# Optimization experiments

Hardware: AMD Instinct MI355X
Metric: run time of the kernel (lower is better)

The kernel has to match this reference:

```python
import jax, jax.numpy as jnp
import numpy as np

BS, S, H, KVH, HD = 4, 4096, 32, 8, 128
BLK = 32                      # tokens per cache page
NB = S // BLK                 # blocks per sequence (128)
NPAGES = BS * NB              # total pages in pool (512)
WIN = 1024                    # sliding window
G = H // KVH                  # query heads per KV head (GQA group)
SCALE = 1.0 / float(np.sqrt(HD))
NEG = -1e30


def setup_inputs() -> dict:
    key = jax.random.key(0)
    k0, k1, k2, k3 = jax.random.split(key, 4)
    q = jax.random.normal(k0, (BS, S, H, HD), dtype=jnp.float32)
    k = jax.random.normal(k1, (BS, S, KVH, HD), dtype=jnp.float32)
    v = jax.random.normal(k2, (BS, S, KVH, HD), dtype=jnp.float32)
    k_cache = jnp.zeros((NPAGES, BLK, KVH, HD), dtype=jnp.float32)
    v_cache = jnp.zeros((NPAGES, BLK, KVH, HD), dtype=jnp.float32)
    # identity block table: page p holds block (p % NB) of sequence (p // NB)
    seq_block_ids = jnp.arange(NPAGES, dtype=jnp.int32).reshape(BS, NB)
    start_positions = jnp.full((BS,), S - 1, dtype=jnp.int32)  # decode last token
    mask = jnp.zeros((BS, 1, 1, S), dtype=jnp.float32)         # additive mask
    sink = jax.random.normal(k3, (H,), dtype=jnp.float32)      # per-head sink logit
    return {"q": q, "k": k, "v": v, "k_cache": k_cache, "v_cache": v_cache,
            "mask": mask, "sink": sink, "seq_block_ids": seq_block_ids,
            "start_positions": start_positions}


def reference(q, k, v, k_cache, v_cache, mask, sink, seq_block_ids, start_positions):
    # ---- prefill: write full k/v into the paged cache ----
    # (the wrapper discards the prefill attention output; cache write is its
    #  only observable effect on the returned decode output)
    kp = k.reshape(BS, NB, BLK, KVH, HD)
    vp = v.reshape(BS, NB, BLK, KVH, HD)
    k_cache = k_cache.at[seq_block_ids].set(kp)
    v_cache = v_cache.at[seq_block_ids].set(vp)

    # ---- decode: write last-token k/v at start_positions ----
    b = jnp.arange(BS)
    pages = seq_block_ids[b, start_positions // BLK]   # [BS]
    offs = start_positions % BLK                       # [BS]
    k_cache = k_cache.at[pages, offs].set(k[:, -1])
    v_cache = v_cache.at[pages, offs].set(v[:, -1])

    # ---- gather cache back into dense [BS, S, KVH, HD] via block table ----
    k_all = k_cache[seq_block_ids].reshape(BS, S, KVH, HD)
    v_all = v_cache[seq_block_ids].reshape(BS, S, KVH, HD)

    # ---- last-token paged attention with sliding window + sink ----
    q_last = q[:, -1].reshape(BS, KVH, G, HD)          # group query heads by KV head
    scores = jnp.einsum('bhgd,bjhd->bhgj', q_last, k_all) * SCALE  # [BS,KVH,G,S]
    scores = scores + mask                              # mask broadcasts over heads
    pos = jnp.arange(S, dtype=jnp.int32)
    p = start_positions[:, None]
    valid = (pos[None, :] <= p) & (p - pos[None, :] < WIN)          # [BS,S]
    scores = jnp.where(valid[:, None, None, :], scores, NEG)

    # softmax with an extra per-head sink logit that contributes no value
    sink_l = sink.reshape(KVH, G)[None, :, :, None]     # [1,KVH,G,1]
    m = jnp.maximum(jnp.max(scores, axis=-1, keepdims=True), sink_l)
    e = jnp.exp(scores - m)
    denom = jnp.sum(e, axis=-1, keepdims=True) + jnp.exp(sink_l - m)
    attn = e / denom                                    # [BS,KVH,G,S]

    out = jnp.einsum('bhgj,bjhd->bhgd', attn, v_all)    # [BS,KVH,G,HD]
    return out.reshape(BS, 1, H, HD)
```

## Files before the change

### kernel.cpp

```cpp
#include <hip/hip_runtime.h>
#include <math.h>

#define BS 4
#define S 4096
#define H 32
#define KVH 8
#define HD 128
#define G 4
#define WIN 1024
#define SCALE 0.08838834764831843f

#define NSPLIT 32
#define CHUNK (WIN / NSPLIT)
#define PSTRIDE 132

#define GLOAD_LDS16(gsrc, ldst) \
    __builtin_amdgcn_global_load_lds( \
        (const __attribute__((address_space(1))) void*)(gsrc), \
        (__attribute__((address_space(3))) void*)(ldst), 16, 0, 0)

__global__ __launch_bounds__(256) void attn_split_kernel(
    const float* __restrict__ q, const float* __restrict__ k,
    const float* __restrict__ v, const float* __restrict__ mask,
    const int* __restrict__ start_positions, float* __restrict__ ws)
{
    const int blk   = blockIdx.x;
    const int split = blk % NSPLIT;
    const int kvh   = (blk / NSPLIT) % KVH;
    const int b     = blk / (NSPLIT * KVH);
    const int tid   = threadIdx.x;
    const int g     = tid >> 6;
    const int lane  = tid & 63;
    const int grp   = lane >> 4;
    const int l16   = lane & 15;
    const int h     = kvh * G + g;

    const int p = start_positions[b];
    const int base_pos = p - WIN + 1 + split * CHUNK;

    __shared__ float kbuf[CHUNK][HD];
    __shared__ float vbuf[CHUNK][HD];
    __shared__ float sc[G][CHUNK];

    const size_t kv_base = (size_t)b * S * (KVH * HD) + (size_t)kvh * HD;

    {
        const int srow = lane >> 5;
        const int scol = (lane & 31) * 4;
        #pragma unroll
        for (int i = 0; i < 4; ++i) {
            const int st  = g * 4 + i;
            const int r   = st * 2 + srow;
            const int pos = base_pos + r;
            const int row = (pos == p) ? (S - 1) : (pos < 0 ? 0 : pos);
            const float* ksrc = k + kv_base + (size_t)row * (KVH * HD) + scol;
            const float* vsrc = v + kv_base + (size_t)row * (KVH * HD) + scol;
            GLOAD_LDS16(ksrc, (char*)&kbuf[0][0] + st * 1024);
            GLOAD_LDS16(vsrc, (char*)&vbuf[0][0] + st * 1024);
        }
    }

    const float* qptr = q + (((size_t)b * S + (S - 1)) * H + h) * HD + l16 * 8;
    const float4 qa = *(const float4*)(qptr);
    const float4 qb = *(const float4*)(qptr + 4);

    __syncthreads();

    #pragma unroll
    for (int it = 0; it < CHUNK / 4; ++it) {
        const int jj  = it * 4 + grp;
        const int pos = base_pos + jj;
        float val = -1e30f;
        const float4 ka = *(const float4*)(&kbuf[jj][l16 * 8]);
        const float4 kb = *(const float4*)(&kbuf[jj][l16 * 8 + 4]);
        if (pos >= 0) {
            float d = qa.x * ka.x + qa.y * ka.y + qa.z * ka.z + qa.w * ka.w
                    + qb.x * kb.x + qb.y * kb.y + qb.z * kb.z + qb.w * kb.w;
            #pragma unroll
            for (int off = 1; off < 16; off <<= 1)
                d += __shfl_xor(d, off, 64);
            val = d * SCALE + mask[(size_t)b * S + pos];
        }
        if (l16 == 0) sc[g][jj] = val;
    }

    const float s_l = sc[g][lane & (CHUNK - 1)];
    float m = s_l;
    #pragma unroll
    for (int off = 1; off < 32; off <<= 1)
        m = fmaxf(m, __shfl_xor(m, off, 64));
    const float e_l = __expf(s_l - m);
    if (lane < CHUNK) sc[g][lane] = e_l;
    float lsum = (lane < CHUNK) ? e_l : 0.f;
    #pragma unroll
    for (int off = 1; off < 64; off <<= 1)
        lsum += __shfl_xor(lsum, off, 64);

    const int half = lane >> 5;
    const int l32  = lane & 31;
    float4 o4 = make_float4(0.f, 0.f, 0.f, 0.f);
    #pragma unroll
    for (int it = 0; it < CHUNK / 2; ++it) {
        const int jj = it * 2 + half;
        const float e = sc[g][jj];
        const float4 v4 = *(const float4*)(&vbuf[jj][l32 * 4]);
        o4.x += e * v4.x; o4.y += e * v4.y; o4.z += e * v4.z; o4.w += e * v4.w;
    }
    o4.x += __shfl_xor(o4.x, 32, 64);
    o4.y += __shfl_xor(o4.y, 32, 64);
    o4.z += __shfl_xor(o4.z, 32, 64);
    o4.w += __shfl_xor(o4.w, 32, 64);

    const size_t widx = ((((size_t)b * KVH + kvh) * G + g) * NSPLIT + split) * (size_t)PSTRIDE;
    if (lane < 32) {
        *(float4*)(ws + widx + 4 * l32) = o4;
        if (lane == 0) { ws[widx + 128] = m; ws[widx + 129] = lsum; }
    }
}

__global__ __launch_bounds__(64) void attn_reduce_kernel(
    const float* __restrict__ ws, const float* __restrict__ sink,
    float* __restrict__ out)
{
    const int blk = blockIdx.x;
    const int h = blk % H;
    const int b = blk / H;
    const int kvh = h / G;
    const int g = h % G;
    const int lane = threadIdx.x;

    const size_t base = ((((size_t)b * KVH + kvh) * G + g) * (size_t)NSPLIT) * (size_t)PSTRIDE;

    const float sk = sink[h];
    float M = sk;
    float ms[NSPLIT];
    #pragma unroll
    for (int s = 0; s < NSPLIT; ++s) {
        ms[s] = ws[base + (size_t)s * PSTRIDE + 128];
        M = fmaxf(M, ms[s]);
    }

    float D = __expf(sk - M);
    float ax = 0.f, ay = 0.f;
    #pragma unroll
    for (int s = 0; s < NSPLIT; ++s) {
        const float w = __expf(ms[s] - M);
        D += w * ws[base + (size_t)s * PSTRIDE + 129];
        const float2 o2 = *(const float2*)(ws + base + (size_t)s * PSTRIDE + 2 * lane);
        ax += w * o2.x;
        ay += w * o2.y;
    }

    const float invD = 1.f / D;
    float2 r; r.x = ax * invD; r.y = ay * invD;
    *(float2*)(out + ((size_t)b * H + h) * HD + 2 * lane) = r;
}

extern "C" void kernel_launch(void* const* d_in, const int* in_sizes, int n_in,
                              void* d_out, int out_size, void* d_ws, size_t ws_size,
                              hipStream_t stream) {
    const float* q    = (const float*)d_in[0];
    const float* k    = (const float*)d_in[1];
    const float* v    = (const float*)d_in[2];
    const float* mask = (const float*)d_in[5];
    const float* sink = (const float*)d_in[6];
    const int* start_positions = (const int*)d_in[8];
    float* out = (float*)d_out;
    float* ws  = (float*)d_ws;

    attn_split_kernel<<<BS * KVH * NSPLIT, 256, 0, stream>>>(q, k, v, mask, start_positions, ws);
    attn_reduce_kernel<<<BS * H, 64, 0, stream>>>(ws, sink, out);
}
```

Measured before the change: 17.56 us.

## Fuse split-K reduce into attention kernel via last-block atomic counter

Merges the split and reduce kernels into one. Each block writes its partial result, bumps a per-(batch, kv-head) atomic counter, and the last block to arrive combines all partials with the sink and writes the output. Counters are zeroed with an async memset before the launch. This removes the second kernel launch and the gap between kernels, at the cost of fences, an atomic and a memset op.

```diff
diff --git a/kernel.cpp b/kernel.cpp
--- a/kernel.cpp
+++ b/kernel.cpp
@@ -13,16 +13,18 @@
 #define NSPLIT 32
 #define CHUNK (WIN / NSPLIT)
 #define PSTRIDE 132
+#define WS_PART_OFF 256
 
 #define GLOAD_LDS16(gsrc, ldst) \
     __builtin_amdgcn_global_load_lds( \
         (const __attribute__((address_space(1))) void*)(gsrc), \
         (__attribute__((address_space(3))) void*)(ldst), 16, 0, 0)
 
-__global__ __launch_bounds__(256) void attn_split_kernel(
+__global__ __launch_bounds__(256) void attn_fused_kernel(
     const float* __restrict__ q, const float* __restrict__ k,
     const float* __restrict__ v, const float* __restrict__ mask,
-    const int* __restrict__ start_positions, float* __restrict__ ws)
+    const float* __restrict__ sink, const int* __restrict__ start_positions,
+    float* __restrict__ ws, float* __restrict__ out)
 {
     const int blk   = blockIdx.x;
     const int split = blk % NSPLIT;
@@ -41,6 +43,7 @@
     __shared__ float kbuf[CHUNK][HD];
     __shared__ float vbuf[CHUNK][HD];
     __shared__ float sc[G][CHUNK];
+    __shared__ int is_last;
 
     const size_t kv_base = (size_t)b * S * (KVH * HD) + (size_t)kvh * HD;
 
@@ -111,25 +114,26 @@
     o4.z += __shfl_xor(o4.z, 32, 64);
     o4.w += __shfl_xor(o4.w, 32, 64);
 
-    const size_t widx = ((((size_t)b * KVH + kvh) * G + g) * NSPLIT + split) * (size_t)PSTRIDE;
+    const size_t widx = WS_PART_OFF +
+        ((((size_t)b * KVH + kvh) * G + g) * NSPLIT + split) * (size_t)PSTRIDE;
     if (lane < 32) {
         *(float4*)(ws + widx + 4 * l32) = o4;
         if (lane == 0) { ws[widx + 128] = m; ws[widx + 129] = lsum; }
     }
-}
 
-__global__ __launch_bounds__(64) void attn_reduce_kernel(
-    const float* __restrict__ ws, const float* __restrict__ sink,
-    float* __restrict__ out)
-{
-    const int blk = blockIdx.x;
-    const int h = blk % H;
-    const int b = blk / H;
-    const int kvh = h / G;
-    const int g = h % G;
-    const int lane = threadIdx.x;
+    __syncthreads();
+    if (tid == 0) {
+        __threadfence();
+        int* cnt = (int*)ws + (b * KVH + kvh);
+        const int old = atomicAdd(cnt, 1);
+        is_last = (old == NSPLIT - 1);
+        if (is_last) __threadfence();
+    }
+    __syncthreads();
+    if (!is_last) return;
 
-    const size_t base = ((((size_t)b * KVH + kvh) * G + g) * (size_t)NSPLIT) * (size_t)PSTRIDE;
+    const size_t base = WS_PART_OFF +
+        ((((size_t)b * KVH + kvh) * G + g) * (size_t)NSPLIT) * (size_t)PSTRIDE;
 
     const float sk = sink[h];
     float M = sk;
@@ -168,6 +172,7 @@
     float* out = (float*)d_out;
     float* ws  = (float*)d_ws;
 
-    attn_split_kernel<<<BS * KVH * NSPLIT, 256, 0, stream>>>(q, k, v, mask, start_positions, ws);
-    attn_reduce_kernel<<<BS * H, 64, 0, stream>>>(ws, sink, out);
+    hipMemsetAsync(d_ws, 0, BS * KVH * sizeof(int), stream);
+    attn_fused_kernel<<<BS * KVH * NSPLIT, 256, 0, stream>>>(
+        q, k, v, mask, sink, start_positions, ws, out);
 }
```

New measurement: 54.14 us. +208.2%, slower.
